# Kernel tuning notes

Hardware: AMD Instinct MI355X
Metric: run time of the kernel (lower is better)

The kernel has to match this reference:

```python
import jax, jax.numpy as jnp
import numpy as np

N_NODES = 50000
N_EDGES = 800000
N_GRAPHS = 64
ALPHA = 0.5
LN_EPS = 1e-5


def _gcn(x, W, b, src, dst, n):
    """GCNConv: h = D^{-1/2}(A+I)D^{-1/2} (x W) + b, edges already include self-loops."""
    h = x @ W                                             # [N, F]
    ones = jnp.ones(src.shape[0], dtype=h.dtype)
    deg = jax.ops.segment_sum(ones, dst, num_segments=n)  # in-degree (target side)
    dinv = jnp.where(deg > 0, jax.lax.rsqrt(deg), 0.0)
    norm = dinv[src] * dinv[dst]                          # [E]
    msg = h[src] * norm[:, None]                          # gather + scale
    return jax.ops.segment_sum(msg, dst, num_segments=n) + b


def _dirgnn(x, W_in, b_in, W_out, b_out, src, dst, n):
    # conv_in on original edges, conv_out on flipped edges; root_weight=False
    x_in = _gcn(x, W_in, b_in, src, dst, n)
    x_out = _gcn(x, W_out, b_out, dst, src, n)
    return ALPHA * x_out + (1.0 - ALPHA) * x_in


def setup_inputs() -> dict:
    key = jax.random.key(0)
    ks = jax.random.split(key, 16)
    d = {}
    d["x"] = jax.random.normal(ks[0], (N_NODES, 64), jnp.float32)
    d["edge_src"] = jax.random.randint(ks[1], (N_EDGES,), 0, N_NODES, jnp.int32)
    d["edge_dst"] = jax.random.randint(ks[2], (N_EDGES,), 0, N_NODES, jnp.int32)
    d["batch"] = jnp.sort(jax.random.randint(ks[3], (N_NODES,), 0, N_GRAPHS, jnp.int32))
    s = 1.0 / np.sqrt(64.0)
    for i, nm in enumerate(["W1_in", "W1_out", "W2_in", "W2_out", "W3_in", "W3_out"]):
        d[nm] = jax.random.normal(ks[4 + i], (64, 64), jnp.float32) * s
        d[nm.replace("W", "b")] = jnp.zeros((64,), jnp.float32)
    d["ln_w"] = jnp.ones((64,), jnp.float32)
    d["ln_b"] = jnp.zeros((64,), jnp.float32)
    d["P1_w"] = jax.random.normal(ks[10], (64, 128), jnp.float32) * s
    d["P1_b"] = jnp.zeros((128,), jnp.float32)
    d["P2_w"] = jax.random.normal(ks[11], (128, 2), jnp.float32) * (1.0 / np.sqrt(128.0))
    d["P2_b"] = jnp.zeros((2,), jnp.float32)
    return d


def reference(x, edge_src, edge_dst, batch,
              W1_in, b1_in, W1_out, b1_out,
              W2_in, b2_in, W2_out, b2_out,
              W3_in, b3_in, W3_out, b3_out,
              ln_w, ln_b, P1_w, P1_b, P2_w, P2_b):
    n = x.shape[0]
    ar = jnp.arange(n, dtype=edge_src.dtype)
    src = jnp.concatenate([edge_src, ar])   # add self-loops once
    dst = jnp.concatenate([edge_dst, ar])

    h = _dirgnn(x, W1_in, b1_in, W1_out, b1_out, src, dst, n)
    h = jax.nn.relu(h)
    h = _dirgnn(h, W2_in, b2_in, W2_out, b2_out, src, dst, n)
    h = jax.nn.relu(h)   # dropout p=0 in eval
    h = _dirgnn(h, W3_in, b3_in, W3_out, b3_out, src, dst, n)

    # global_mean_pool over graphs
    sums = jax.ops.segment_sum(h, batch, num_segments=N_GRAPHS)
    cnt = jax.ops.segment_sum(jnp.ones((n,), h.dtype), batch, num_segments=N_GRAPHS)
    pooled = sums / jnp.maximum(cnt, 1.0)[:, None]        # [G, 64]

    # LayerNorm
    mu = jnp.mean(pooled, axis=-1, keepdims=True)
    var = jnp.mean(jnp.square(pooled - mu), axis=-1, keepdims=True)
    z = (pooled - mu) * jax.lax.rsqrt(var + LN_EPS) * ln_w + ln_b

    z = jax.nn.relu(z @ P1_w + P1_b)
    return z @ P2_w + P2_b                                 # [G, 2]
```

## Files before the change

### kernel.cpp

```cpp
#include <hip/hip_runtime.h>

#define N_NODES 50000
#define N_EDGES 800000
#define N_GRAPHS 64
#define LN_EPS 1e-5f
#define NPAD 50176
#define NXCD 8
#define NODES_PER_GRP (N_NODES / NXCD)
#define BIN_CAP 103000
#define BPGB 64
#define NBLK_BIN 512
#define CHUNK_BIN 1563


__global__ __launch_bounds__(256) void init_kernel(int* deg_in, int* deg_out,
                                                   int* gc, float* pool_sum, int* cnt) {
    int i = blockIdx.x * 256 + threadIdx.x;
    if (i < N_NODES) { deg_in[i] = 1; deg_out[i] = 1; }
    if (i < 2) gc[i] = 0;
    if (i < N_GRAPHS * 64) pool_sum[i] = 0.f;
    if (i < N_GRAPHS) cnt[i] = 0;
}

__global__ __launch_bounds__(256) void bin_count_kernel(
    const int* __restrict__ src, const int* __restrict__ dst,
    int* __restrict__ blockHist) {
    __shared__ int h[16];
    if (threadIdx.x < 16) h[threadIdx.x] = 0;
    __syncthreads();
    const int e0 = blockIdx.x * CHUNK_BIN;
    const int e1 = min(e0 + CHUNK_BIN, N_EDGES);
    for (int e = e0 + threadIdx.x; e < e1; e += 256) {
        atomicAdd(&h[dst[e] / NODES_PER_GRP], 1);
        atomicAdd(&h[8 + src[e] / NODES_PER_GRP], 1);
    }
    __syncthreads();
    if (threadIdx.x < 16) blockHist[blockIdx.x * 16 + threadIdx.x] = h[threadIdx.x];
}

__global__ __launch_bounds__(1024) void bin_scan_kernel(
    const int* __restrict__ blockHist, int* __restrict__ off, int* __restrict__ binCnt) {
    const int b = threadIdx.x >> 6;
    const int lane = threadIdx.x & 63;
    int v[8]; int loc = 0;
#pragma unroll
    for (int k = 0; k < 8; ++k) {
        v[k] = blockHist[(lane * 8 + k) * 16 + b];
        loc += v[k];
    }
    int s = loc;
#pragma unroll
    for (int o = 1; o < 64; o <<= 1) {
        int t = __shfl_up(s, o);
        if (lane >= o) s += t;
    }
    int excl = s - loc;
#pragma unroll
    for (int k = 0; k < 8; ++k) {
        off[(lane * 8 + k) * 16 + b] = excl;
        excl += v[k];
    }
    if (lane == 63) binCnt[b] = s;
}

__global__ __launch_bounds__(256) void bin_scatter_kernel(
    const int* __restrict__ src, const int* __restrict__ dst,
    const int* __restrict__ off,
    int2* __restrict__ binIn, int2* __restrict__ binOut) {
    __shared__ int h[16];
    if (threadIdx.x < 16) h[threadIdx.x] = off[blockIdx.x * 16 + threadIdx.x];
    __syncthreads();
    const int e0 = blockIdx.x * CHUNK_BIN;
    const int e1 = min(e0 + CHUNK_BIN, N_EDGES);
    for (int e = e0 + threadIdx.x; e < e1; e += 256) {
        int d = dst[e], s = src[e];
        int gd = d / NODES_PER_GRP, gs = s / NODES_PER_GRP;
        int p = atomicAdd(&h[gd], 1);
        binIn[(size_t)gd * BIN_CAP + p] = make_int2(d, s);
        int q = atomicAdd(&h[8 + gs], 1);
        binOut[(size_t)gs * BIN_CAP + q] = make_int2(s, d);
    }
}

__global__ __launch_bounds__(256) void degree_bin_kernel(
    const int* __restrict__ binCnt,
    const int2* __restrict__ binIn, const int2* __restrict__ binOut,
    int* deg_in, int* deg_out) {
    const int g = blockIdx.x & (NXCD - 1);
    const int sub = blockIdx.x >> 3;
    const int stride = BPGB * 256;
    {
        const int n = binCnt[g];
        for (int i = sub * 256 + threadIdx.x; i < n; i += stride)
            atomicAdd(&deg_in[binIn[(size_t)g * BIN_CAP + i].x], 1);
    }
    {
        const int n = binCnt[NXCD + g];
        for (int i = sub * 256 + threadIdx.x; i < n; i += stride)
            atomicAdd(&deg_out[binOut[(size_t)g * BIN_CAP + i].x], 1);
    }
}

__global__ __launch_bounds__(256) void prep_kernel(
    const int* __restrict__ deg_in, const int* __restrict__ deg_out,
    float* __restrict__ dinv_in, float* __restrict__ dinv_out,
    int* __restrict__ base_in, int* __restrict__ base_out,
    int* __restrict__ cur_in, int* __restrict__ cur_out, int* gc) {
    __shared__ int lws[4];
    const int i = blockIdx.x * 256 + threadIdx.x;
    const int tid = threadIdx.x, lane = tid & 63, wid = tid >> 6;

#pragma unroll
    for (int dir = 0; dir < 2; ++dir) {
        const int* deg = dir ? deg_out : deg_in;
        float* dinv    = dir ? dinv_out : dinv_in;
        int* base      = dir ? base_out : base_in;
        int* cur       = dir ? cur_out : cur_in;
        int d = (i < N_NODES) ? deg[i] : 1;
        if (i < N_NODES) dinv[i] = rsqrtf((float)d);
        int v = d - 1;
        int s = v;
#pragma unroll
        for (int off = 1; off < 64; off <<= 1) {
            int t = __shfl_up(s, off);
            if (lane >= off) s += t;
        }
        if (lane == 63) lws[wid] = s;
        __syncthreads();
        if (tid == 0) {
            int tmp[4]; int tot = 0;
            for (int w = 0; w < 4; ++w) { tmp[w] = tot; tot += lws[w]; }
            int bb = atomicAdd(&gc[dir], tot);
            for (int w = 0; w < 4; ++w) lws[w] = bb + tmp[w];
        }
        __syncthreads();
        int b = lws[wid] + s - v;
        if (i < N_NODES) { base[i] = b; cur[i] = b; }
        __syncthreads();
    }
}

__global__ __launch_bounds__(256) void place_bin_kernel(
    const int* __restrict__ binCnt,
    const int2* __restrict__ binIn, const int2* __restrict__ binOut,
    int* cur_in, int* cur_out,
    int* __restrict__ csr_in, int* __restrict__ csr_out) {
    const int g = blockIdx.x & (NXCD - 1);
    const int sub = blockIdx.x >> 3;
    const int stride = BPGB * 256;
    {
        const int n = binCnt[g];
        for (int i = sub * 256 + threadIdx.x; i < n; i += stride) {
            int2 ed = binIn[(size_t)g * BIN_CAP + i];
            int p = atomicAdd(&cur_in[ed.x], 1);
            csr_in[p] = ed.y;
        }
    }
    {
        const int n = binCnt[NXCD + g];
        for (int i = sub * 256 + threadIdx.x; i < n; i += stride) {
            int2 ed = binOut[(size_t)g * BIN_CAP + i];
            int q = atomicAdd(&cur_out[ed.x], 1);
            csr_out[q] = ed.y;
        }
    }
}

__global__ __launch_bounds__(256) void aggregate_kernel(
    const float* __restrict__ act,
    const int* __restrict__ deg_in, const int* __restrict__ deg_out,
    const float* __restrict__ dinv_in, const float* __restrict__ dinv_out,
    const int* __restrict__ base_in, const int* __restrict__ base_out,
    const int* __restrict__ csr_in, const int* __restrict__ csr_out,
    float* __restrict__ AggIn, float* __restrict__ AggOut) {
    int node = (blockIdx.x << 2) + (threadIdx.x >> 6);
    if (node >= N_NODES) return;
    const int lane = threadIdx.x & 63;
    const float di = dinv_in[node];
    const float dq = dinv_out[node];
    const float self = act[(size_t)node * 64 + lane];
    float sumI = 0.f, sumO = 0.f;
    {
        const int b = base_in[node];
        const int n = deg_in[node] - 1;
        int j = 0;
        for (; j + 8 <= n; j += 8) {
            int s0 = __builtin_amdgcn_readfirstlane(csr_in[b + j]);
            int s1 = __builtin_amdgcn_readfirstlane(csr_in[b + j + 1]);
            int s2 = __builtin_amdgcn_readfirstlane(csr_in[b + j + 2]);
            int s3 = __builtin_amdgcn_readfirstlane(csr_in[b + j + 3]);
            int s4 = __builtin_amdgcn_readfirstlane(csr_in[b + j + 4]);
            int s5 = __builtin_amdgcn_readfirstlane(csr_in[b + j + 5]);
            int s6 = __builtin_amdgcn_readfirstlane(csr_in[b + j + 6]);
            int s7 = __builtin_amdgcn_readfirstlane(csr_in[b + j + 7]);
            float w0 = dinv_in[s0], w1 = dinv_in[s1], w2 = dinv_in[s2], w3 = dinv_in[s3];
            float w4 = dinv_in[s4], w5 = dinv_in[s5], w6 = dinv_in[s6], w7 = dinv_in[s7];
            float v0 = act[(size_t)s0 * 64 + lane];
            float v1 = act[(size_t)s1 * 64 + lane];
            float v2 = act[(size_t)s2 * 64 + lane];
            float v3 = act[(size_t)s3 * 64 + lane];
            float v4 = act[(size_t)s4 * 64 + lane];
            float v5 = act[(size_t)s5 * 64 + lane];
            float v6 = act[(size_t)s6 * 64 + lane];
            float v7 = act[(size_t)s7 * 64 + lane];
            sumI += (w0 * v0 + w1 * v1 + w2 * v2 + w3 * v3)
                  + (w4 * v4 + w5 * v5 + w6 * v6 + w7 * v7);
        }
        for (; j < n; ++j) {
            int s0 = __builtin_amdgcn_readfirstlane(csr_in[b + j]);
            sumI += dinv_in[s0] * act[(size_t)s0 * 64 + lane];
        }
    }
    {
        const int b = base_out[node];
        const int n = deg_out[node] - 1;
        int j = 0;
        for (; j + 8 <= n; j += 8) {
            int s0 = __builtin_amdgcn_readfirstlane(csr_out[b + j]);
            int s1 = __builtin_amdgcn_readfirstlane(csr_out[b + j + 1]);
            int s2 = __builtin_amdgcn_readfirstlane(csr_out[b + j + 2]);
            int s3 = __builtin_amdgcn_readfirstlane(csr_out[b + j + 3]);
            int s4 = __builtin_amdgcn_readfirstlane(csr_out[b + j + 4]);
            int s5 = __builtin_amdgcn_readfirstlane(csr_out[b + j + 5]);
            int s6 = __builtin_amdgcn_readfirstlane(csr_out[b + j + 6]);
            int s7 = __builtin_amdgcn_readfirstlane(csr_out[b + j + 7]);
            float w0 = dinv_out[s0], w1 = dinv_out[s1], w2 = dinv_out[s2], w3 = dinv_out[s3];
            float w4 = dinv_out[s4], w5 = dinv_out[s5], w6 = dinv_out[s6], w7 = dinv_out[s7];
            float v0 = act[(size_t)s0 * 64 + lane];
            float v1 = act[(size_t)s1 * 64 + lane];
            float v2 = act[(size_t)s2 * 64 + lane];
            float v3 = act[(size_t)s3 * 64 + lane];
            float v4 = act[(size_t)s4 * 64 + lane];
            float v5 = act[(size_t)s5 * 64 + lane];
            float v6 = act[(size_t)s6 * 64 + lane];
            float v7 = act[(size_t)s7 * 64 + lane];
            sumO += (w0 * v0 + w1 * v1 + w2 * v2 + w3 * v3)
                  + (w4 * v4 + w5 * v5 + w6 * v6 + w7 * v7);
        }
        for (; j < n; ++j) {
            int s0 = __builtin_amdgcn_readfirstlane(csr_out[b + j]);
            sumO += dinv_out[s0] * act[(size_t)s0 * 64 + lane];
        }
    }
    AggIn[(size_t)node * 64 + lane]  = di * (di * self + sumI);
    AggOut[(size_t)node * 64 + lane] = dq * (dq * self + sumO);
}

__global__ __launch_bounds__(256) void gemm_combine_kernel(
    const float* __restrict__ Ain, const float* __restrict__ Aout,
    const float* __restrict__ Win, const float* __restrict__ Wout,
    const float* __restrict__ b_in, const float* __restrict__ b_out,
    float* __restrict__ act, int do_relu) {
    __shared__ __align__(16) float sWin[64 * 64];
    __shared__ __align__(16) float sWout[64 * 64];
    __shared__ __align__(16) float sAin[64 * 68];
    __shared__ __align__(16) float sAout[64 * 68];
    const int tx = threadIdx.x;
    for (int i = tx * 4; i < 4096; i += 1024) {
        *(float4*)&sWin[i]  = *(const float4*)&Win[i];
        *(float4*)&sWout[i] = *(const float4*)&Wout[i];
    }
    const int row0 = blockIdx.x * 64;
    for (int i = tx; i < 1024; i += 256) {
        int r = i >> 4;
        int k4 = (i & 15) << 2;
        int gr = row0 + r;
        float4 vi = make_float4(0.f, 0.f, 0.f, 0.f);
        float4 vo = vi;
        if (gr < N_NODES) {
            vi = *(const float4*)&Ain[(size_t)gr * 64 + k4];
            vo = *(const float4*)&Aout[(size_t)gr * 64 + k4];
        }
        *(float4*)&sAin[r * 68 + k4]  = vi;
        *(float4*)&sAout[r * 68 + k4] = vo;
    }
    __syncthreads();
    const int ct = tx & 15;
    const int rg = tx >> 4;
    const int c4 = ct << 2;
    float aI[4][4], aO[4][4];
#pragma unroll
    for (int i = 0; i < 4; ++i)
#pragma unroll
        for (int j = 0; j < 4; ++j) { aI[i][j] = 0.f; aO[i][j] = 0.f; }
#pragma unroll 4
    for (int k0 = 0; k0 < 64; k0 += 4) {
        float4 avI[4], avO[4];
#pragma unroll
        for (int i = 0; i < 4; ++i) {
            avI[i] = *(float4*)&sAin[(rg * 4 + i) * 68 + k0];
            avO[i] = *(float4*)&sAout[(rg * 4 + i) * 68 + k0];
        }
#pragma unroll
        for (int kk = 0; kk < 4; ++kk) {
            float4 wi = *(float4*)&sWin[(k0 + kk) * 64 + c4];
            float4 wo = *(float4*)&sWout[(k0 + kk) * 64 + c4];
#pragma unroll
            for (int i = 0; i < 4; ++i) {
                float ai = (&avI[i].x)[kk];
                float ao = (&avO[i].x)[kk];
                aI[i][0] += ai * wi.x; aI[i][1] += ai * wi.y;
                aI[i][2] += ai * wi.z; aI[i][3] += ai * wi.w;
                aO[i][0] += ao * wo.x; aO[i][1] += ao * wo.y;
                aO[i][2] += ao * wo.z; aO[i][3] += ao * wo.w;
            }
        }
    }
    float4 bi = *(const float4*)&b_in[c4];
    float4 bo = *(const float4*)&b_out[c4];
#pragma unroll
    for (int i = 0; i < 4; ++i) {
        int gr = row0 + rg * 4 + i;
        if (gr < N_NODES) {
            float4 r;
            r.x = 0.5f * (aO[i][0] + bo.x) + 0.5f * (aI[i][0] + bi.x);
            r.y = 0.5f * (aO[i][1] + bo.y) + 0.5f * (aI[i][1] + bi.y);
            r.z = 0.5f * (aO[i][2] + bo.z) + 0.5f * (aI[i][2] + bi.z);
            r.w = 0.5f * (aO[i][3] + bo.w) + 0.5f * (aI[i][3] + bi.w);
            if (do_relu) {
                r.x = fmaxf(r.x, 0.f); r.y = fmaxf(r.y, 0.f);
                r.z = fmaxf(r.z, 0.f); r.w = fmaxf(r.w, 0.f);
            }
            *(float4*)&act[(size_t)gr * 64 + c4] = r;
        }
    }
}

__global__ __launch_bounds__(256) void pool_kernel(
    const float* __restrict__ h, const int* __restrict__ batch,
    float* __restrict__ pool_sum, int* __restrict__ cnt) {
    int w = (blockIdx.x << 2) + (threadIdx.x >> 6);
    int n0 = w << 5;
    if (n0 >= N_NODES) return;
    const int lane = threadIdx.x & 63;
    int n1 = min(n0 + 32, N_NODES);
    int g = batch[n0];
    float acc = 0.f;
    int run = 0;
    for (int nn = n0; nn < n1; ++nn) {
        int bg = batch[nn];
        if (bg != g) {
            unsafeAtomicAdd(&pool_sum[g * 64 + lane], acc);
            if (lane == 0) atomicAdd(&cnt[g], run);
            acc = 0.f; run = 0; g = bg;
        }
        acc += h[(size_t)nn * 64 + lane];
        run++;
    }
    unsafeAtomicAdd(&pool_sum[g * 64 + lane], acc);
    if (lane == 0) atomicAdd(&cnt[g], run);
}

__global__ __launch_bounds__(64) void head_kernel(
    const float* __restrict__ pool_sum, const int* __restrict__ cnt,
    const float* __restrict__ ln_w, const float* __restrict__ ln_b,
    const float* __restrict__ P1w, const float* __restrict__ P1b,
    const float* __restrict__ P2w, const float* __restrict__ P2b,
    float* __restrict__ out) {
    __shared__ float zbuf[64];
    const int g = blockIdx.x, f = threadIdx.x;
    float c = fmaxf((float)cnt[g], 1.0f);
    float p = pool_sum[g * 64 + f] / c;
    float s = p;
#pragma unroll
    for (int o = 32; o >= 1; o >>= 1) s += __shfl_xor(s, o);
    float mu = s * (1.0f / 64.0f);
    float dv = p - mu;
    float q = dv * dv;
#pragma unroll
    for (int o = 32; o >= 1; o >>= 1) q += __shfl_xor(q, o);
    float var = q * (1.0f / 64.0f);
    float z = dv * rsqrtf(var + LN_EPS) * ln_w[f] + ln_b[f];
    zbuf[f] = z;
    __syncthreads();
    float s0 = 0.f, s1 = 0.f;
#pragma unroll 8
    for (int k = 0; k < 64; ++k) {
        float zk = zbuf[k];
        s0 += zk * P1w[k * 128 + f];
        s1 += zk * P1w[k * 128 + f + 64];
    }
    float r0 = fmaxf(s0 + P1b[f], 0.f);
    float r1 = fmaxf(s1 + P1b[f + 64], 0.f);
    float p0 = r0 * P2w[f * 2 + 0] + r1 * P2w[(f + 64) * 2 + 0];
    float p1 = r0 * P2w[f * 2 + 1] + r1 * P2w[(f + 64) * 2 + 1];
#pragma unroll
    for (int o = 32; o >= 1; o >>= 1) {
        p0 += __shfl_xor(p0, o);
        p1 += __shfl_xor(p1, o);
    }
    if (f == 0) {
        out[g * 2 + 0] = p0 + P2b[0];
        out[g * 2 + 1] = p1 + P2b[1];
    }
}

extern "C" void kernel_launch(void* const* d_in, const int* in_sizes, int n_in,
                              void* d_out, int out_size, void* d_ws, size_t ws_size,
                              hipStream_t stream) {
    const float* x     = (const float*)d_in[0];
    const int* esrc    = (const int*)d_in[1];
    const int* edst    = (const int*)d_in[2];
    const int* batch   = (const int*)d_in[3];
    const float* W1_in  = (const float*)d_in[4];
    const float* b1_in  = (const float*)d_in[5];
    const float* W1_out = (const float*)d_in[6];
    const float* b1_out = (const float*)d_in[7];
    const float* W2_in  = (const float*)d_in[8];
    const float* b2_in  = (const float*)d_in[9];
    const float* W2_out = (const float*)d_in[10];
    const float* b2_out = (const float*)d_in[11];
    const float* W3_in  = (const float*)d_in[12];
    const float* b3_in  = (const float*)d_in[13];
    const float* W3_out = (const float*)d_in[14];
    const float* b3_out = (const float*)d_in[15];
    const float* ln_w  = (const float*)d_in[16];
    const float* ln_b  = (const float*)d_in[17];
    const float* P1w   = (const float*)d_in[18];
    const float* P1b   = (const float*)d_in[19];
    const float* P2w   = (const float*)d_in[20];
    const float* P2b   = (const float*)d_in[21];
    float* out = (float*)d_out;

    float* ws = (float*)d_ws;
    const size_t NF = (size_t)N_NODES * 64;
    int*   deg_in   = (int*)(ws + 0 * NPAD);
    int*   deg_out  = (int*)(ws + 1 * NPAD);
    float* dinv_in  = ws + 2 * NPAD;
    float* dinv_out = ws + 3 * NPAD;
    int*   base_in  = (int*)(ws + 4 * NPAD);
    int*   base_out = (int*)(ws + 5 * NPAD);
    int*   cur_in   = (int*)(ws + 6 * NPAD);
    int*   cur_out  = (int*)(ws + 7 * NPAD);
    int*   small    = (int*)(ws + 8 * NPAD);
    int*   gc       = small;
    int*   binCnt   = small + 2;
    float* pool_sum = ws + 8 * NPAD + 64;
    int*   cnt      = (int*)(ws + 8 * NPAD + 64 + 4096);
    int*   blockHist= small + 4224;
    int*   boff     = small + 4224 + 8192;
    float* act      = ws + 9 * NPAD;
    float* AggIn    = act + NF;
    float* AggOut   = AggIn + NF;
    int*   csr_in   = (int*)(AggOut + NF);
    int*   csr_out  = csr_in + N_EDGES;
    int2*  binIn    = (int2*)AggIn;
    int2*  binOut   = (int2*)AggOut;

    const int nblk = (N_NODES + 255) / 256;
    init_kernel<<<nblk, 256, 0, stream>>>(deg_in, deg_out, gc, pool_sum, cnt);
    bin_count_kernel<<<NBLK_BIN, 256, 0, stream>>>(esrc, edst, blockHist);
    bin_scan_kernel<<<1, 1024, 0, stream>>>(blockHist, boff, binCnt);
    bin_scatter_kernel<<<NBLK_BIN, 256, 0, stream>>>(esrc, edst, boff, binIn, binOut);
    degree_bin_kernel<<<NXCD * BPGB, 256, 0, stream>>>(binCnt, binIn, binOut,
                                                       deg_in, deg_out);
    prep_kernel<<<nblk, 256, 0, stream>>>(deg_in, deg_out, dinv_in, dinv_out,
                                          base_in, base_out, cur_in, cur_out, gc);
    place_bin_kernel<<<NXCD * BPGB, 256, 0, stream>>>(binCnt, binIn, binOut,
                                                      cur_in, cur_out, csr_in, csr_out);

    const int agg_grid  = (N_NODES + 3) / 4;
    const int gemm_grid = (N_NODES + 63) / 64;

    aggregate_kernel<<<agg_grid, 256, 0, stream>>>(x, deg_in, deg_out, dinv_in, dinv_out,
                                                   base_in, base_out, csr_in, csr_out,
                                                   AggIn, AggOut);
    gemm_combine_kernel<<<gemm_grid, 256, 0, stream>>>(AggIn, AggOut, W1_in, W1_out,
                                                       b1_in, b1_out, act, 1);
    aggregate_kernel<<<agg_grid, 256, 0, stream>>>(act, deg_in, deg_out, dinv_in, dinv_out,
                                                   base_in, base_out, csr_in, csr_out,
                                                   AggIn, AggOut);
    gemm_combine_kernel<<<gemm_grid, 256, 0, stream>>>(AggIn, AggOut, W2_in, W2_out,
                                                       b2_in, b2_out, act, 1);
    aggregate_kernel<<<agg_grid, 256, 0, stream>>>(act, deg_in, deg_out, dinv_in, dinv_out,
                                                   base_in, base_out, csr_in, csr_out,
                                                   AggIn, AggOut);
    gemm_combine_kernel<<<gemm_grid, 256, 0, stream>>>(AggIn, AggOut, W3_in, W3_out,
                                                       b3_in, b3_out, act, 0);

    pool_kernel<<<(N_NODES + 127) / 128, 256, 0, stream>>>(act, batch, pool_sum, cnt);
    head_kernel<<<N_GRAPHS, 64, 0, stream>>>(pool_sum, cnt, ln_w, ln_b, P1w, P1b, P2w, P2b, out);
}
```

Before: 553.5 us.

## Fuse neighbor aggregation with dual GEMM into one per-layer kernel

Merges the aggregate and gemm_combine kernels into a single 512-thread kernel. Each wavefront gathers 8 node rows into shared memory, then the block runs the 64x64 in/out GEMMs with bias, the alpha combine and ReLU. This removes the write and re-read of the AggIn/AggOut intermediates and halves the number of launches per layer. In exchange, activations ping-pong between two buffers, the edge bins move to their own workspace region, and per-block gather imbalance now delays the GEMM phase of that block.

```diff
diff --git a/kernel.cpp b/kernel.cpp
--- a/kernel.cpp
+++ b/kernel.cpp
@@ -166,137 +166,103 @@
     }
 }
 
-__global__ __launch_bounds__(256) void aggregate_kernel(
-    const float* __restrict__ act,
+__device__ __forceinline__ float gather_dir(
+    const float* __restrict__ act, const float* __restrict__ dinv,
+    const int* __restrict__ csr, int b, int n, int lane) {
+    float sum = 0.f;
+    int j = 0;
+    for (; j + 8 <= n; j += 8) {
+        int s0 = __builtin_amdgcn_readfirstlane(csr[b + j]);
+        int s1 = __builtin_amdgcn_readfirstlane(csr[b + j + 1]);
+        int s2 = __builtin_amdgcn_readfirstlane(csr[b + j + 2]);
+        int s3 = __builtin_amdgcn_readfirstlane(csr[b + j + 3]);
+        int s4 = __builtin_amdgcn_readfirstlane(csr[b + j + 4]);
+        int s5 = __builtin_amdgcn_readfirstlane(csr[b + j + 5]);
+        int s6 = __builtin_amdgcn_readfirstlane(csr[b + j + 6]);
+        int s7 = __builtin_amdgcn_readfirstlane(csr[b + j + 7]);
+        float w0 = dinv[s0], w1 = dinv[s1], w2 = dinv[s2], w3 = dinv[s3];
+        float w4 = dinv[s4], w5 = dinv[s5], w6 = dinv[s6], w7 = dinv[s7];
+        float v0 = act[(size_t)s0 * 64 + lane];
+        float v1 = act[(size_t)s1 * 64 + lane];
+        float v2 = act[(size_t)s2 * 64 + lane];
+        float v3 = act[(size_t)s3 * 64 + lane];
+        float v4 = act[(size_t)s4 * 64 + lane];
+        float v5 = act[(size_t)s5 * 64 + lane];
+        float v6 = act[(size_t)s6 * 64 + lane];
+        float v7 = act[(size_t)s7 * 64 + lane];
+        sum += (w0 * v0 + w1 * v1 + w2 * v2 + w3 * v3)
+             + (w4 * v4 + w5 * v5 + w6 * v6 + w7 * v7);
+    }
+    for (; j < n; ++j) {
+        int s0 = __builtin_amdgcn_readfirstlane(csr[b + j]);
+        sum += dinv[s0] * act[(size_t)s0 * 64 + lane];
+    }
+    return sum;
+}
+
+__global__ __launch_bounds__(512) void fused_layer_kernel(
+    const float* __restrict__ src_act,
     const int* __restrict__ deg_in, const int* __restrict__ deg_out,
     const float* __restrict__ dinv_in, const float* __restrict__ dinv_out,
     const int* __restrict__ base_in, const int* __restrict__ base_out,
     const int* __restrict__ csr_in, const int* __restrict__ csr_out,
-    float* __restrict__ AggIn, float* __restrict__ AggOut) {
-    int node = (blockIdx.x << 2) + (threadIdx.x >> 6);
-    if (node >= N_NODES) return;
-    const int lane = threadIdx.x & 63;
-    const float di = dinv_in[node];
-    const float dq = dinv_out[node];
-    const float self = act[(size_t)node * 64 + lane];
-    float sumI = 0.f, sumO = 0.f;
-    {
-        const int b = base_in[node];
-        const int n = deg_in[node] - 1;
-        int j = 0;
-        for (; j + 8 <= n; j += 8) {
-            int s0 = __builtin_amdgcn_readfirstlane(csr_in[b + j]);
-            int s1 = __builtin_amdgcn_readfirstlane(csr_in[b + j + 1]);
-            int s2 = __builtin_amdgcn_readfirstlane(csr_in[b + j + 2]);
-            int s3 = __builtin_amdgcn_readfirstlane(csr_in[b + j + 3]);
-            int s4 = __builtin_amdgcn_readfirstlane(csr_in[b + j + 4]);
-            int s5 = __builtin_amdgcn_readfirstlane(csr_in[b + j + 5]);
-            int s6 = __builtin_amdgcn_readfirstlane(csr_in[b + j + 6]);
-            int s7 = __builtin_amdgcn_readfirstlane(csr_in[b + j + 7]);
-            float w0 = dinv_in[s0], w1 = dinv_in[s1], w2 = dinv_in[s2], w3 = dinv_in[s3];
-            float w4 = dinv_in[s4], w5 = dinv_in[s5], w6 = dinv_in[s6], w7 = dinv_in[s7];
-            float v0 = act[(size_t)s0 * 64 + lane];
-            float v1 = act[(size_t)s1 * 64 + lane];
-            float v2 = act[(size_t)s2 * 64 + lane];
-            float v3 = act[(size_t)s3 * 64 + lane];
-            float v4 = act[(size_t)s4 * 64 + lane];
-            float v5 = act[(size_t)s5 * 64 + lane];
-            float v6 = act[(size_t)s6 * 64 + lane];
-            float v7 = act[(size_t)s7 * 64 + lane];
-            sumI += (w0 * v0 + w1 * v1 + w2 * v2 + w3 * v3)
-                  + (w4 * v4 + w5 * v5 + w6 * v6 + w7 * v7);
-        }
-        for (; j < n; ++j) {
-            int s0 = __builtin_amdgcn_readfirstlane(csr_in[b + j]);
-            sumI += dinv_in[s0] * act[(size_t)s0 * 64 + lane];
-        }
-    }
-    {
-        const int b = base_out[node];
-        const int n = deg_out[node] - 1;
-        int j = 0;
-        for (; j + 8 <= n; j += 8) {
-            int s0 = __builtin_amdgcn_readfirstlane(csr_out[b + j]);
-            int s1 = __builtin_amdgcn_readfirstlane(csr_out[b + j + 1]);
-            int s2 = __builtin_amdgcn_readfirstlane(csr_out[b + j + 2]);
-            int s3 = __builtin_amdgcn_readfirstlane(csr_out[b + j + 3]);
-            int s4 = __builtin_amdgcn_readfirstlane(csr_out[b + j + 4]);
-            int s5 = __builtin_amdgcn_readfirstlane(csr_out[b + j + 5]);
-            int s6 = __builtin_amdgcn_readfirstlane(csr_out[b + j + 6]);
-            int s7 = __builtin_amdgcn_readfirstlane(csr_out[b + j + 7]);
-            float w0 = dinv_out[s0], w1 = dinv_out[s1], w2 = dinv_out[s2], w3 = dinv_out[s3];
-            float w4 = dinv_out[s4], w5 = dinv_out[s5], w6 = dinv_out[s6], w7 = dinv_out[s7];
-            float v0 = act[(size_t)s0 * 64 + lane];
-            float v1 = act[(size_t)s1 * 64 + lane];
-            float v2 = act[(size_t)s2 * 64 + lane];
-            float v3 = act[(size_t)s3 * 64 + lane];
-            float v4 = act[(size_t)s4 * 64 + lane];
-            float v5 = act[(size_t)s5 * 64 + lane];
-            float v6 = act[(size_t)s6 * 64 + lane];
-            float v7 = act[(size_t)s7 * 64 + lane];
-            sumO += (w0 * v0 + w1 * v1 + w2 * v2 + w3 * v3)
-                  + (w4 * v4 + w5 * v5 + w6 * v6 + w7 * v7);
-        }
-        for (; j < n; ++j) {
-            int s0 = __builtin_amdgcn_readfirstlane(csr_out[b + j]);
-            sumO += dinv_out[s0] * act[(size_t)s0 * 64 + lane];
-        }
-    }
-    AggIn[(size_t)node * 64 + lane]  = di * (di * self + sumI);
-    AggOut[(size_t)node * 64 + lane] = dq * (dq * self + sumO);
-}
-
-__global__ __launch_bounds__(256) void gemm_combine_kernel(
-    const float* __restrict__ Ain, const float* __restrict__ Aout,
     const float* __restrict__ Win, const float* __restrict__ Wout,
     const float* __restrict__ b_in, const float* __restrict__ b_out,
-    float* __restrict__ act, int do_relu) {
-    __shared__ __align__(16) float sWin[64 * 64];
-    __shared__ __align__(16) float sWout[64 * 64];
+    float* __restrict__ dst_act, int do_relu) {
+    __shared__ __align__(16) float sWin[4096];
+    __shared__ __align__(16) float sWout[4096];
     __shared__ __align__(16) float sAin[64 * 68];
     __shared__ __align__(16) float sAout[64 * 68];
     const int tx = threadIdx.x;
-    for (int i = tx * 4; i < 4096; i += 1024) {
+    for (int i = tx * 4; i < 4096; i += 2048) {
         *(float4*)&sWin[i]  = *(const float4*)&Win[i];
         *(float4*)&sWout[i] = *(const float4*)&Wout[i];
     }
+    const int lane = tx & 63;
+    const int wv = tx >> 6;
     const int row0 = blockIdx.x * 64;
-    for (int i = tx; i < 1024; i += 256) {
-        int r = i >> 4;
-        int k4 = (i & 15) << 2;
-        int gr = row0 + r;
-        float4 vi = make_float4(0.f, 0.f, 0.f, 0.f);
-        float4 vo = vi;
-        if (gr < N_NODES) {
-            vi = *(const float4*)&Ain[(size_t)gr * 64 + k4];
-            vo = *(const float4*)&Aout[(size_t)gr * 64 + k4];
-        }
-        *(float4*)&sAin[r * 68 + k4]  = vi;
-        *(float4*)&sAout[r * 68 + k4] = vo;
+#pragma unroll 1
+    for (int i = 0; i < 8; ++i) {
+        const int r = wv * 8 + i;
+        const int node = row0 + r;
+        float aI = 0.f, aO = 0.f;
+        if (node < N_NODES) {
+            const float di = dinv_in[node];
+            const float dq = dinv_out[node];
+            const float self = src_act[(size_t)node * 64 + lane];
+            float sumI = gather_dir(src_act, dinv_in, csr_in,
+                                    base_in[node], deg_in[node] - 1, lane);
+            float sumO = gather_dir(src_act, dinv_out, csr_out,
+                                    base_out[node], deg_out[node] - 1, lane);
+            aI = di * (di * self + sumI);
+            aO = dq * (dq * self + sumO);
+        }
+        sAin[r * 68 + lane]  = aI;
+        sAout[r * 68 + lane] = aO;
     }
     __syncthreads();
     const int ct = tx & 15;
     const int rg = tx >> 4;
     const int c4 = ct << 2;
-    float aI[4][4], aO[4][4];
-#pragma unroll
-    for (int i = 0; i < 4; ++i)
+    float aI[2][4], aO[2][4];
+#pragma unroll
+    for (int i = 0; i < 2; ++i)
 #pragma unroll
         for (int j = 0; j < 4; ++j) { aI[i][j] = 0.f; aO[i][j] = 0.f; }
 #pragma unroll 4
     for (int k0 = 0; k0 < 64; k0 += 4) {
-        float4 avI[4], avO[4];
-#pragma unroll
-        for (int i = 0; i < 4; ++i) {
-            avI[i] = *(float4*)&sAin[(rg * 4 + i) * 68 + k0];
-            avO[i] = *(float4*)&sAout[(rg * 4 + i) * 68 + k0];
+        float4 avI[2], avO[2];
+#pragma unroll
+        for (int i = 0; i < 2; ++i) {
+            avI[i] = *(float4*)&sAin[(rg * 2 + i) * 68 + k0];
+            avO[i] = *(float4*)&sAout[(rg * 2 + i) * 68 + k0];
         }
 #pragma unroll
         for (int kk = 0; kk < 4; ++kk) {
             float4 wi = *(float4*)&sWin[(k0 + kk) * 64 + c4];
             float4 wo = *(float4*)&sWout[(k0 + kk) * 64 + c4];
 #pragma unroll
-            for (int i = 0; i < 4; ++i) {
+            for (int i = 0; i < 2; ++i) {
                 float ai = (&avI[i].x)[kk];
                 float ao = (&avO[i].x)[kk];
                 aI[i][0] += ai * wi.x; aI[i][1] += ai * wi.y;
@@ -309,8 +275,8 @@
     float4 bi = *(const float4*)&b_in[c4];
     float4 bo = *(const float4*)&b_out[c4];
 #pragma unroll
-    for (int i = 0; i < 4; ++i) {
-        int gr = row0 + rg * 4 + i;
+    for (int i = 0; i < 2; ++i) {
+        int gr = row0 + rg * 2 + i;
         if (gr < N_NODES) {
             float4 r;
             r.x = 0.5f * (aO[i][0] + bo.x) + 0.5f * (aI[i][0] + bi.x);
@@ -321,7 +287,7 @@
                 r.x = fmaxf(r.x, 0.f); r.y = fmaxf(r.y, 0.f);
                 r.z = fmaxf(r.z, 0.f); r.w = fmaxf(r.w, 0.f);
             }
-            *(float4*)&act[(size_t)gr * 64 + c4] = r;
+            *(float4*)&dst_act[(size_t)gr * 64 + c4] = r;
         }
     }
 }
@@ -439,13 +405,12 @@
     int*   cnt      = (int*)(ws + 8 * NPAD + 64 + 4096);
     int*   blockHist= small + 4224;
     int*   boff     = small + 4224 + 8192;
-    float* act      = ws + 9 * NPAD;
-    float* AggIn    = act + NF;
-    float* AggOut   = AggIn + NF;
-    int*   csr_in   = (int*)(AggOut + NF);
+    float* actA     = ws + 9 * NPAD;
+    float* actB     = actA + NF;
+    int*   csr_in   = (int*)(actB + NF);
     int*   csr_out  = csr_in + N_EDGES;
-    int2*  binIn    = (int2*)AggIn;
-    int2*  binOut   = (int2*)AggOut;
+    int2*  binIn    = (int2*)(csr_out + N_EDGES);
+    int2*  binOut   = binIn + (size_t)NXCD * BIN_CAP;
 
     const int nblk = (N_NODES + 255) / 256;
     init_kernel<<<nblk, 256, 0, stream>>>(deg_in, deg_out, gc, pool_sum, cnt);
@@ -459,25 +424,18 @@
     place_bin_kernel<<<NXCD * BPGB, 256, 0, stream>>>(binCnt, binIn, binOut,
                                                       cur_in, cur_out, csr_in, csr_out);
 
-    const int agg_grid  = (N_NODES + 3) / 4;
-    const int gemm_grid = (N_NODES + 63) / 64;
-
-    aggregate_kernel<<<agg_grid, 256, 0, stream>>>(x, deg_in, deg_out, dinv_in, dinv_out,
-                                                   base_in, base_out, csr_in, csr_out,
-                                                   AggIn, AggOut);
-    gemm_combine_kernel<<<gemm_grid, 256, 0, stream>>>(AggIn, AggOut, W1_in, W1_out,
-                                                       b1_in, b1_out, act, 1);
-    aggregate_kernel<<<agg_grid, 256, 0, stream>>>(act, deg_in, deg_out, dinv_in, dinv_out,
-                                                   base_in, base_out, csr_in, csr_out,
-                                                   AggIn, AggOut);
-    gemm_combine_kernel<<<gemm_grid, 256, 0, stream>>>(AggIn, AggOut, W2_in, W2_out,
-                                                       b2_in, b2_out, act, 1);
-    aggregate_kernel<<<agg_grid, 256, 0, stream>>>(act, deg_in, deg_out, dinv_in, dinv_out,
-                                                   base_in, base_out, csr_in, csr_out,
-                                                   AggIn, AggOut);
-    gemm_combine_kernel<<<gemm_grid, 256, 0, stream>>>(AggIn, AggOut, W3_in, W3_out,
-                                                       b3_in, b3_out, act, 0);
-
-    pool_kernel<<<(N_NODES + 127) / 128, 256, 0, stream>>>(act, batch, pool_sum, cnt);
+    const int fuse_grid = (N_NODES + 63) / 64;
+
+    fused_layer_kernel<<<fuse_grid, 512, 0, stream>>>(x, deg_in, deg_out,
+        dinv_in, dinv_out, base_in, base_out, csr_in, csr_out,
+        W1_in, W1_out, b1_in, b1_out, actA, 1);
+    fused_layer_kernel<<<fuse_grid, 512, 0, stream>>>(actA, deg_in, deg_out,
+        dinv_in, dinv_out, base_in, base_out, csr_in, csr_out,
+        W2_in, W2_out, b2_in, b2_out, actB, 1);
+    fused_layer_kernel<<<fuse_grid, 512, 0, stream>>>(actB, deg_in, deg_out,
+        dinv_in, dinv_out, base_in, base_out, csr_in, csr_out,
+        W3_in, W3_out, b3_in, b3_out, actA, 0);
+
+    pool_kernel<<<(N_NODES + 127) / 128, 256, 0, stream>>>(actA, batch, pool_sum, cnt);
     head_kernel<<<N_GRAPHS, 64, 0, stream>>>(pool_sum, cnt, ln_w, ln_b, P1w, P1b, P2w, P2b, out);
 }
```

Result: slower. 954.1 us (+72.4%).
